# Performance work log

Hardware: AMD Instinct MI355X
Metric: run time of the kernel (lower is better)

The kernel has to match this reference:

```python
import jax, jax.numpy as jnp
import numpy as np

TAU = 1.0
EPS = 1e-5


def _gcn_sparse(x, src, dst, ew, W, b, n):
    # PyG GCNConv: add self-loops (weight 1), sym-normalize, aggregate src->dst
    deg = jax.ops.segment_sum(ew, dst, num_segments=n) + 1.0
    dinv = jnp.where(deg > 0, jax.lax.rsqrt(deg), 0.0)
    h = x @ W
    coef = dinv[src] * ew * dinv[dst]              # [E]
    out = jax.ops.segment_sum(h[src] * coef[:, None], dst, num_segments=n)
    out = out + h * (dinv * dinv)[:, None]         # self-loop term
    return out + b


def _gcn_dense(x, A, W, b):
    # x: [B,N,d], A: [B,N,N] with A[b,i,j] = weight of edge j->i
    n = A.shape[-1]
    Ah = A + jnp.eye(n, dtype=A.dtype)
    deg = Ah.sum(-1)
    dinv = jnp.where(deg > 0, jax.lax.rsqrt(deg), 0.0)
    An = dinv[:, :, None] * Ah * dinv[:, None, :]
    return jnp.einsum('bij,bjd->bid', An, x @ W) + b


def _bn_silu(x, g, be, axes):
    # BatchNorm over node axis (training-mode batch stats, biased var) + SiLU
    m = x.mean(axes, keepdims=True)
    v = x.var(axes, keepdims=True)
    return jax.nn.silu(g * (x - m) * jax.lax.rsqrt(v + EPS) + be)


def setup_inputs() -> dict:
    key = jax.random.key(0)
    ks = jax.random.split(key, 12)
    B, NPG, EPER = 32, 1024, 16384
    CIN, C, K1, K2, OUT = 64, 128, 128, 32, 10
    N, E = B * NPG, B * EPER
    ei = jax.random.randint(ks[0], (2, E), 0, NPG, dtype=jnp.int32)
    off = jnp.repeat(jnp.arange(B, dtype=jnp.int32) * NPG, EPER)
    edge_index = ei + off[None, :]
    x = jax.random.normal(ks[1], (N, CIN), jnp.float32)
    batch = jnp.repeat(jnp.arange(B, dtype=jnp.int32), NPG)
    batch_ptr = jnp.arange(B + 1, dtype=jnp.int32) * NPG
    p = lambda k, s: jax.random.normal(k, s, jnp.float32) * 0.05
    return dict(
        x=x, edge_index=edge_index, batch=batch, batch_ptr=batch_ptr,
        w1a=p(ks[2], (CIN, C)), b1a=jnp.zeros((C,)), g1a=jnp.ones((C,)), be1a=jnp.zeros((C,)),
        w1b=p(ks[3], (C, C)), b1b=jnp.zeros((C,)), g1b=jnp.ones((C,)), be1b=jnp.zeros((C,)),
        wp1=p(ks[4], (C, K1)), bp1=jnp.zeros((K1,)),
        w2a=p(ks[5], (C, C)), b2a=jnp.zeros((C,)), g2a=jnp.ones((C,)), be2a=jnp.zeros((C,)),
        w2b=p(ks[6], (C, C)), b2b=jnp.zeros((C,)), g2b=jnp.ones((C,)), be2b=jnp.zeros((C,)),
        wp2=p(ks[7], (C, K2)), bp2=jnp.zeros((K2,)),
        wl=p(ks[8], (C, OUT)), bl=jnp.zeros((OUT,)))


def reference(x, edge_index, batch, batch_ptr,
              w1a, b1a, g1a, be1a, w1b, b1b, g1b, be1b, wp1, bp1,
              w2a, b2a, g2a, be2a, w2b, b2b, g2b, be2b, wp2, bp2,
              wl, bl):
    n = x.shape[0]
    B = batch_ptr.shape[0] - 1
    npg = n // B                                    # uniform nodes per graph
    src, dst = edge_index[0], edge_index[1]
    ew = jnp.ones((edge_index.shape[1],), x.dtype)  # edge_weight=None -> ones

    # ---- stack 1: sparse GCN residual blocks + stochastic pool ----
    h = _bn_silu(_gcn_sparse(x, src, dst, ew, w1a, b1a, n), g1a, be1a, 0)
    h = h + _bn_silu(_gcn_sparse(h, src, dst, ew, w1b, b1b, n), g1b, be1b, 0)
    s = jax.nn.softmax(_gcn_sparse(h, src, dst, ew, wp1, bp1, n) / TAU, -1)  # [n,K1]
    s3 = s.reshape(B, npg, -1)
    x2 = jnp.einsum('bnc,bnd->bcd', s3, h.reshape(B, npg, -1))   # s^T x  [B,K1,C]
    t = jax.ops.segment_sum(s[src] * ew[:, None], dst, num_segments=n)  # A s
    A2 = jnp.einsum('bnc,bnk->bck', s3, t.reshape(B, npg, -1))   # s^T A s [B,K1,K1]

    # ---- stack 2: dense GCN on pooled graph + stochastic pool ----
    h2 = _bn_silu(_gcn_dense(x2, A2, w2a, b2a), g2a, be2a, (0, 1))
    h2 = h2 + _bn_silu(_gcn_dense(h2, A2, w2b, b2b), g2b, be2b, (0, 1))
    s2 = jax.nn.softmax(_gcn_dense(h2, A2, wp2, bp2) / TAU, -1)  # [B,K1,K2]
    x3 = jnp.einsum('bnc,bnd->bcd', s2, h2)                      # [B,K2,C]

    # global mean pool over nodes per graph, linear, log_softmax
    g = x3.mean(axis=1)
    out = jax.nn.log_softmax(g @ wl + bl, axis=1)
    # aux losses are multiplied by 0 in the original forward -> exact zero
    return (out, jnp.zeros((), x.dtype))
```

## Files before the change

kernel.cpp:

```cpp
#include <hip/hip_runtime.h>
#include <cmath>

#define KSPLIT 8
#define ELL_ST 80

typedef __attribute__((ext_vector_type(8))) short short8;
typedef __attribute__((ext_vector_type(4))) float float4v;

static __device__ __forceinline__ unsigned short f2bf(float f){
  union { float f; unsigned u; } c; c.f = f;
  unsigned r = c.u + 0x7fff + ((c.u >> 16) & 1);
  return (unsigned short)(r >> 16);
}
static __device__ __forceinline__ float u2f(unsigned u){
  union { unsigned u; float f; } c; c.u = u; return c.f;
}
static __device__ __forceinline__ float silu(float y){ return y/(1.f+__expf(-y)); }

static __device__ __forceinline__ void coef_prologue(const float* __restrict__ stats,
                                                     const float* __restrict__ gamma,
                                                     const float* __restrict__ beta,
                                                     float invM, float* lds, int tbase){
  int t = threadIdx.x - tbase;
  if(t >= 0 && t < 128){
    float s = 0.f, q = 0.f;
    #pragma unroll
    for(int k=0;k<8;k++){ s += stats[k*128+t]; q += stats[1024 + k*128+t]; }
    float m = s*invM;
    float v = q*invM - m*m;
    float sc = gamma[t]*rsqrtf(v + 1e-5f);
    lds[t] = sc;
    lds[128+t] = beta[t] - m*sc;
  }
}

__global__ void k_fill_wt(const int* __restrict__ src, const int* __restrict__ dst,
                          int* __restrict__ cursor, int* __restrict__ esrc, int E,
                          const float* __restrict__ w1a, const float* __restrict__ w1b,
                          const float* __restrict__ wp1, unsigned short* __restrict__ t1a,
                          unsigned short* __restrict__ t1b, unsigned short* __restrict__ tp1,
                          int CIN){
  int i = blockIdx.x*256 + threadIdx.x;
  if(i < E){
    int d = dst[i];
    int p = atomicAdd(&cursor[d], 1);
    if(p < ELL_ST) esrc[(size_t)d*ELL_ST + p] = src[i];
  } else {
    int j = i - E;
    int n1 = CIN*128, n2 = 128*128;
    if(j >= 0 && j < n1){
      int k = j >> 7, c = j & 127;
      t1a[(size_t)c*CIN + k] = f2bf(w1a[j]);
    } else if(j >= n1 && j < n1+n2){
      int jj = j - n1; int k = jj >> 7, c = jj & 127;
      t1b[(size_t)c*128 + k] = f2bf(w1b[jj]);
    } else if(j >= n1+n2 && j < n1+2*n2){
      int jj = j - n1 - n2; int k = jj >> 7, c = jj & 127;
      tp1[(size_t)c*128 + k] = f2bf(wp1[jj]);
    }
  }
}

__global__ void k_gemm_mfma(const float* __restrict__ A, const float* __restrict__ A2,
                            const unsigned short* __restrict__ Bt,
                            unsigned short* __restrict__ Cb,
                            unsigned short* __restrict__ Hout, int M, int K,
                            const int* __restrict__ rowdeg,
                            const float* __restrict__ stA, const float* __restrict__ gA,
                            const float* __restrict__ beA,
                            const float* __restrict__ stB, const float* __restrict__ gB,
                            const float* __restrict__ beB, float invM){
  __shared__ unsigned short Abf[64][40];
  __shared__ unsigned short Bbf[128][40];
  __shared__ float lcA[256], lcB[256];
  int tid = threadIdx.x;
  if(stA) coef_prologue(stA, gA, beA, invM, lcA, 0);
  if(stB) coef_prologue(stB, gB, beB, invM, lcB, 128);
  if(stA || stB) __syncthreads();
  int wv = tid >> 6, lane = tid & 63;
  int quad = lane >> 4, l16 = lane & 15;
  int row0 = blockIdx.x*64;
  int sr = tid >> 2, sk = (tid & 3)*8;
  int srb = tid >> 1, skb = (tid & 1)*16;
  float4v acc[8] = {};
  for(int kt=0; kt<K; kt+=32){
    const float* ap = &A[(size_t)(row0+sr)*K + kt + sk];
    float va[8];
    *(float4*)&va[0] = *(const float4*)ap;
    *(float4*)&va[4] = *(const float4*)(ap+4);
    if(stB){
      const float* bp = &A2[(size_t)(row0+sr)*K + kt + sk];
      float vb[8];
      *(float4*)&vb[0] = *(const float4*)bp;
      *(float4*)&vb[4] = *(const float4*)(bp+4);
      #pragma unroll
      for(int i=0;i<8;i++){
        int c = kt+sk+i;
        va[i] = silu(lcA[c]*va[i] + lcA[128+c]) + silu(lcB[c]*vb[i] + lcB[128+c]);
      }
    } else if(stA){
      #pragma unroll
      for(int i=0;i<8;i++){
        int c = kt+sk+i;
        va[i] = silu(lcA[c]*va[i] + lcA[128+c]);
      }
    }
    uint4 pk;
    pk.x = (unsigned)f2bf(va[0]) | ((unsigned)f2bf(va[1])<<16);
    pk.y = (unsigned)f2bf(va[2]) | ((unsigned)f2bf(va[3])<<16);
    pk.z = (unsigned)f2bf(va[4]) | ((unsigned)f2bf(va[5])<<16);
    pk.w = (unsigned)f2bf(va[6]) | ((unsigned)f2bf(va[7])<<16);
    *(uint4*)&Abf[sr][sk] = pk;
    if(Hout)
      *(uint4*)&Hout[(size_t)(row0+sr)*128 + kt + sk] = pk;
    *(uint4*)&Bbf[srb][skb]   = *(const uint4*)&Bt[(size_t)srb*K + kt + skb];
    *(uint4*)&Bbf[srb][skb+8] = *(const uint4*)&Bt[(size_t)srb*K + kt + skb + 8];
    __syncthreads();
    short8 af = *(const short8*)&Abf[wv*16 + l16][quad*8];
    #pragma unroll
    for(int t=0;t<8;t++){
      short8 bf = *(const short8*)&Bbf[t*16 + l16][quad*8];
      acc[t] = __builtin_amdgcn_mfma_f32_16x16x32_bf16(af, bf, acc[t], 0, 0, 0);
    }
    __syncthreads();
  }
  float scr[4];
  #pragma unroll
  for(int r=0;r<4;r++){
    int grow = row0 + wv*16 + quad*4 + r;
    scr[r] = rowdeg ? rsqrtf((float)rowdeg[grow] + 1.0f) : 1.f;
  }
  #pragma unroll
  for(int t=0;t<8;t++){
    #pragma unroll
    for(int r=0;r<4;r++){
      int grow = row0 + wv*16 + quad*4 + r;
      Cb[(size_t)grow*128 + t*16 + l16] = f2bf(acc[t][r]*scr[r]);
    }
  }
}

__global__ void k_gemm64(const float* __restrict__ A, const float* __restrict__ B,
                         float* __restrict__ C, int M, int K, int Nc,
                         const float* __restrict__ rowscale,
                         const float* __restrict__ stA, const float* __restrict__ gA,
                         const float* __restrict__ beA, float invM){
  __shared__ float As[16][68];
  __shared__ float Bs[16][68];
  __shared__ float lc[256];
  int tid = threadIdx.x;
  if(stA){ coef_prologue(stA, gA, beA, invM, lc, 0); __syncthreads(); }
  int tx = tid & 15, ty = tid >> 4;
  int row0 = blockIdx.y*64, col0 = blockIdx.x*64;
  float acc[4][4] = {};
  for(int kt=0; kt<K; kt+=16){
    int ra = tid >> 2, ka = (tid & 3)*4;
    float4 va = *(const float4*)&A[(size_t)(row0+ra)*K + kt + ka];
    if(stA){
      float vv[4] = {va.x, va.y, va.z, va.w};
      #pragma unroll
      for(int i=0;i<4;i++){
        int c = kt+ka+i;
        vv[i] = silu(lc[c]*vv[i] + lc[128+c]);
      }
      va.x=vv[0]; va.y=vv[1]; va.z=vv[2]; va.w=vv[3];
    }
    As[ka+0][ra]=va.x; As[ka+1][ra]=va.y; As[ka+2][ra]=va.z; As[ka+3][ra]=va.w;
    int rb = tid >> 4, cb = (tid & 15)*4;
    *(float4*)&Bs[rb][cb] = *(const float4*)&B[(size_t)(kt+rb)*Nc + col0 + cb];
    __syncthreads();
    #pragma unroll
    for(int k=0;k<16;k++){
      float4 a = *(const float4*)&As[k][ty*4];
      float4 b = *(const float4*)&Bs[k][tx*4];
      float av[4]={a.x,a.y,a.z,a.w}, bv[4]={b.x,b.y,b.z,b.w};
      #pragma unroll
      for(int i=0;i<4;i++)
        #pragma unroll
        for(int j=0;j<4;j++) acc[i][j] += av[i]*bv[j];
    }
    __syncthreads();
  }
  #pragma unroll
  for(int i=0;i<4;i++){
    int r = row0 + ty*4 + i;
    float sc = rowscale ? rowscale[r] : 1.0f;
    float4 v; v.x=acc[i][0]*sc; v.y=acc[i][1]*sc; v.z=acc[i][2]*sc; v.w=acc[i][3]*sc;
    *(float4*)&C[(size_t)r*Nc + col0 + tx*4] = v;
  }
}

template<bool DO_SOFTMAX, bool GCN, bool STATS, bool BF16IN, bool BF16OUT>
__global__ void k_gather(const int* __restrict__ degc, const int* __restrict__ esrc,
                         const void* __restrict__ hWs,
                         const float* __restrict__ bias, float* __restrict__ out,
                         float* __restrict__ stats){
  __shared__ float lsum[4][128];
  __shared__ float lsq[4][128];
  const unsigned short* h16 = (const unsigned short*)hWs;
  const float* h32 = (const float*)hWs;
  int wave = threadIdx.x >> 6;
  int lane = threadIdx.x & 63;
  int bid = blockIdx.x;
  int d = ((bid & 7) << 12) | ((bid >> 3) << 2) | wave;
  int grp = lane >> 5;
  int c4 = (lane & 31)*4;
  int dgr = degc[d];
  int cnt = dgr > ELL_ST ? ELL_ST : dgr;
  cnt = __builtin_amdgcn_readfirstlane(cnt);
  const int* row = esrc + (size_t)d*ELL_ST;

  auto loadrow = [&](int s)->float4{
    if(BF16IN){
      uint2 u = *(const uint2*)&h16[(size_t)s*128 + c4];
      float4 v;
      v.x = u2f(u.x << 16); v.y = u2f(u.x & 0xffff0000u);
      v.z = u2f(u.y << 16); v.w = u2f(u.y & 0xffff0000u);
      return v;
    } else {
      return *(const float4*)&h32[(size_t)s*128 + c4];
    }
  };

  float4 a0 = {0.f,0.f,0.f,0.f}, a1 = {0.f,0.f,0.f,0.f};
  float4 a2 = {0.f,0.f,0.f,0.f}, a3 = {0.f,0.f,0.f,0.f};
  if(GCN && grp == 0)
    a0 = loadrow(d);
  for(int base=0; base<cnt; base+=32){
    int m = cnt - base; if(m > 32) m = 32;
    int idx = (lane < m) ? row[base + lane] : 0;
    int full = m & ~7;
    int j0 = 0;
    for(; j0 < full; j0 += 8){
      int s0 = __shfl(idx, j0+grp);
      int s1 = __shfl(idx, j0+grp+2);
      int s2 = __shfl(idx, j0+grp+4);
      int s3 = __shfl(idx, j0+grp+6);
      float4 v0 = loadrow(s0);
      float4 v1 = loadrow(s1);
      float4 v2 = loadrow(s2);
      float4 v3 = loadrow(s3);
      a0.x+=v0.x; a0.y+=v0.y; a0.z+=v0.z; a0.w+=v0.w;
      a1.x+=v1.x; a1.y+=v1.y; a1.z+=v1.z; a1.w+=v1.w;
      a2.x+=v2.x; a2.y+=v2.y; a2.z+=v2.z; a2.w+=v2.w;
      a3.x+=v3.x; a3.y+=v3.y; a3.z+=v3.z; a3.w+=v3.w;
    }
    if(j0 < m){
      int jj0 = j0+grp, jj1 = j0+grp+2, jj2 = j0+grp+4, jj3 = j0+grp+6;
      int s0 = __shfl(idx, jj0 < m ? jj0 : 0);
      int s1 = __shfl(idx, jj1 < m ? jj1 : 0);
      int s2 = __shfl(idx, jj2 < m ? jj2 : 0);
      int s3 = __shfl(idx, jj3 < m ? jj3 : 0);
      if(jj0 < m){ float4 v = loadrow(s0);
        a0.x+=v.x; a0.y+=v.y; a0.z+=v.z; a0.w+=v.w; }
      if(jj1 < m){ float4 v = loadrow(s1);
        a1.x+=v.x; a1.y+=v.y; a1.z+=v.z; a1.w+=v.w; }
      if(jj2 < m){ float4 v = loadrow(s2);
        a2.x+=v.x; a2.y+=v.y; a2.z+=v.z; a2.w+=v.w; }
      if(jj3 < m){ float4 v = loadrow(s3);
        a3.x+=v.x; a3.y+=v.y; a3.z+=v.z; a3.w+=v.w; }
    }
  }
  float4 acc;
  acc.x = (a0.x+a1.x)+(a2.x+a3.x);
  acc.y = (a0.y+a1.y)+(a2.y+a3.y);
  acc.z = (a0.z+a1.z)+(a2.z+a3.z);
  acc.w = (a0.w+a1.w)+(a2.w+a3.w);
  acc.x += __shfl_xor(acc.x, 32);
  acc.y += __shfl_xor(acc.y, 32);
  acc.z += __shfl_xor(acc.z, 32);
  acc.w += __shfl_xor(acc.w, 32);
  float4 val = acc;
  if(GCN){
    float dv = rsqrtf((float)dgr + 1.0f);
    float4 bi = *(const float4*)&bias[c4];
    val.x = dv*acc.x + bi.x; val.y = dv*acc.y + bi.y;
    val.z = dv*acc.z + bi.z; val.w = dv*acc.w + bi.w;
  }
  if(DO_SOFTMAX){
    float mx = fmaxf(fmaxf(val.x,val.y), fmaxf(val.z,val.w));
    #pragma unroll
    for(int o=1;o<32;o<<=1) mx = fmaxf(mx, __shfl_xor(mx,o));
    float4 e; e.x=__expf(val.x-mx); e.y=__expf(val.y-mx);
    e.z=__expf(val.z-mx); e.w=__expf(val.w-mx);
    float s = e.x+e.y+e.z+e.w;
    #pragma unroll
    for(int o=1;o<32;o<<=1) s += __shfl_xor(s,o);
    float inv = 1.f/s;
    val.x=e.x*inv; val.y=e.y*inv; val.z=e.z*inv; val.w=e.w*inv;
  }
  if(grp == 0){
    if(BF16OUT){
      unsigned short* o16 = (unsigned short*)out;
      uint2 w;
      w.x = (unsigned)f2bf(val.x) | ((unsigned)f2bf(val.y)<<16);
      w.y = (unsigned)f2bf(val.z) | ((unsigned)f2bf(val.w)<<16);
      *(uint2*)&o16[(size_t)d*128 + c4] = w;
    } else {
      *(float4*)&out[(size_t)d*128 + c4] = val;
    }
  }
  if(STATS){
    if(grp == 0){
      *(float4*)&lsum[wave][c4] = val;
      float4 q; q.x=val.x*val.x; q.y=val.y*val.y; q.z=val.z*val.z; q.w=val.w*val.w;
      *(float4*)&lsq[wave][c4] = q;
    }
    __syncthreads();
    int t = threadIdx.x;
    if(t < 128){
      float s = (lsum[0][t]+lsum[1][t]) + (lsum[2][t]+lsum[3][t]);
      atomicAdd(&stats[(bid & 7)*128 + t], s);
    } else {
      int c = t - 128;
      float q = (lsq[0][c]+lsq[1][c]) + (lsq[2][c]+lsq[3][c]);
      atomicAdd(&stats[1024 + (bid & 7)*128 + c], q);
    }
  }
}

__global__ __launch_bounds__(256, 2)
void k_pool2(const unsigned short* __restrict__ P, const unsigned short* __restrict__ QH,
             const unsigned short* __restrict__ QT,
             float* __restrict__ part1, float* __restrict__ part2, int npg, int nb){
  __shared__ unsigned short sT[128][40];
  __shared__ unsigned short qT[128][40];
  int tid = threadIdx.x;
  bool zq = (blockIdx.z == 0);
  const unsigned short* Q = zq ? QH : QT;
  int ks = blockIdx.x, b = blockIdx.y;
  int klen = npg / KSPLIT;
  size_t base = ((size_t)b*npg + (size_t)ks*klen)*128;
  int wv = tid >> 6, lane = tid & 63;
  int quad = lane >> 4, l16 = lane & 15;
  int wr = (wv >> 1)*64, wc = (wv & 1)*64;
  int arr = tid >> 7;
  int t7 = tid & 127;
  int sg = (t7 >> 4)*16;
  int sr2 = (t7 & 15)*2;
  float4v acc[4][4] = {};

  for(int c0 = 0; c0 < klen; c0 += 32){
    size_t i0 = base + (size_t)(c0+sr2)*128 + sg;
    const unsigned short* Sp = arr ? Q : P;
    unsigned short (*dstT)[40] = arr ? qT : sT;
    uint4 ua = *(const uint4*)&Sp[i0];
    uint4 ub = *(const uint4*)&Sp[i0+8];
    uint4 uc = *(const uint4*)&Sp[i0+128];
    uint4 ud = *(const uint4*)&Sp[i0+136];
    unsigned short lo[16], hi[16];
    *(uint4*)&lo[0]=ua; *(uint4*)&lo[8]=ub;
    *(uint4*)&hi[0]=uc; *(uint4*)&hi[8]=ud;
    #pragma unroll
    for(int j=0;j<16;j++)
      *(unsigned*)&dstT[sg+j][sr2] = (unsigned)lo[j] | ((unsigned)hi[j]<<16);
    __syncthreads();
    #pragma unroll
    for(int i=0;i<4;i++){
      short8 af = *(const short8*)&sT[wr + i*16 + l16][quad*8];
      #pragma unroll
      for(int j=0;j<4;j++){
        short8 bf = *(const short8*)&qT[wc + j*16 + l16][quad*8];
        acc[i][j] = __builtin_amdgcn_mfma_f32_16x16x32_bf16(af, bf, acc[i][j], 0, 0, 0);
      }
    }
    __syncthreads();
  }

  float* outp = (zq ? part1 : part2) + ((size_t)(ks*nb + b)*128)*128;
  #pragma unroll
  for(int i=0;i<4;i++)
    #pragma unroll
    for(int r=0;r<4;r++){
      int m = wr + i*16 + quad*4 + r;
      #pragma unroll
      for(int j=0;j<4;j++)
        outp[(size_t)m*128 + wc + j*16 + l16] = acc[i][j][r];
    }
}

__global__ void k_pool_reduce2(const float* __restrict__ p1, const float* __restrict__ p2,
                               float* __restrict__ x2, float* __restrict__ A2,
                               float* __restrict__ dinv2, int total){
  int i = blockIdx.x*256 + threadIdx.x;
  int half = total >> 2;
  if(i < half){
    float4 s = *(const float4*)&p1[(size_t)i*4];
    #pragma unroll
    for(int ks=1; ks<KSPLIT; ks++){
      float4 v = *(const float4*)&p1[(size_t)ks*total + (size_t)i*4];
      s.x+=v.x; s.y+=v.y; s.z+=v.z; s.w+=v.w;
    }
    *(float4*)&x2[(size_t)i*4] = s;
  } else {
    int ia = i - half;
    float4 s = *(const float4*)&p2[(size_t)ia*4];
    #pragma unroll
    for(int ks=1; ks<KSPLIT; ks++){
      float4 v = *(const float4*)&p2[(size_t)ks*total + (size_t)ia*4];
      s.x+=v.x; s.y+=v.y; s.z+=v.z; s.w+=v.w;
    }
    *(float4*)&A2[(size_t)ia*4] = s;
    float rs = s.x+s.y+s.z+s.w;
    #pragma unroll
    for(int o=16;o>0;o>>=1) rs += __shfl_xor(rs, o);
    if((threadIdx.x & 31) == 0) dinv2[ia>>5] = rsqrtf(rs + 1.0f);
  }
}

__global__ void k_bgemm_post_stats(const float* __restrict__ A, const float* __restrict__ X,
                                   const float* __restrict__ dinv2, const float* __restrict__ bias,
                                   float* __restrict__ outp, float* __restrict__ stats){
  __shared__ float As[16][17], Xs[16][17];
  __shared__ float rs[16][17], rq[16][17];
  int b = blockIdx.z;
  int i0 = blockIdx.y*16, j0 = blockIdx.x*16;
  int tx = threadIdx.x, ty = threadIdx.y;
  const float* Ab = A + (size_t)b*16384;
  const float* Xb = X + (size_t)b*16384;
  float acc = 0.f;
  for(int k0=0;k0<128;k0+=16){
    As[ty][tx] = Ab[(i0+ty)*128 + k0+tx];
    Xs[ty][tx] = Xb[(k0+ty)*128 + j0+tx];
    __syncthreads();
    #pragma unroll
    for(int k=0;k<16;k++) acc += As[ty][k]*Xs[k][tx];
    __syncthreads();
  }
  int gr = b*128 + i0 + ty;
  float v = dinv2[gr]*(acc + Xb[(i0+ty)*128 + j0+tx]) + bias[j0+tx];
  outp[(size_t)gr*128 + j0+tx] = v;
  rs[ty][tx] = v; rq[ty][tx] = v*v;
  __syncthreads();
  if(ty == 0){
    float s = 0.f, q = 0.f;
    #pragma unroll
    for(int k=0;k<16;k++){ s += rs[k][tx]; q += rq[k][tx]; }
    int slot = b & 7;
    atomicAdd(&stats[slot*128 + j0+tx], s);
    atomicAdd(&stats[1024 + slot*128 + j0+tx], q);
  }
}

__global__ void k_final(const float* __restrict__ dTa, const float* __restrict__ dTb,
                        const float* __restrict__ stA, const float* __restrict__ gA,
                        const float* __restrict__ beA,
                        const float* __restrict__ stB, const float* __restrict__ gB,
                        const float* __restrict__ beB, float invMc,
                        const float* __restrict__ wl, const float* __restrict__ bl,
                        float* __restrict__ out, int K1n, int Cc, float inv_k2,
                        int OUTc, int zero_idx){
  __shared__ float lcA[256], lcB[256];
  __shared__ float red[256];
  __shared__ float gsh[128];
  __shared__ float logits[32];
  __shared__ float mred, lred;
  coef_prologue(stA, gA, beA, invMc, lcA, 0);
  coef_prologue(stB, gB, beB, invMc, lcB, 128);
  __syncthreads();
  int b = blockIdx.x;
  int tid = threadIdx.x;
  int c = tid & 127, rh = tid >> 7;
  const float* pa = dTa + (size_t)b*K1n*Cc;
  const float* pb = dTb + (size_t)b*K1n*Cc;
  float sa = lcA[c], ha = lcA[128+c], sb = lcB[c], hb = lcB[128+c];
  float acc = 0.f;
  for(int r = rh; r < K1n; r += 2){
    float ya = sa*pa[(size_t)r*Cc + c] + ha;
    float yb = sb*pb[(size_t)r*Cc + c] + hb;
    acc += silu(ya) + silu(yb);
  }
  red[tid] = acc;
  __syncthreads();
  if(tid < 128) gsh[tid] = (red[tid] + red[tid+128]) * inv_k2;
  __syncthreads();
  if(tid < OUTc){
    float l = bl[tid];
    for(int d=0; d<Cc; d++) l += gsh[d]*wl[d*OUTc + tid];
    logits[tid] = l;
  }
  __syncthreads();
  if(tid==0){
    float m = -1e30f;
    for(int o=0;o<OUTc;o++) m = fmaxf(m, logits[o]);
    float s = 0.f;
    for(int o=0;o<OUTc;o++) s += __expf(logits[o]-m);
    mred = m; lred = logf(s);
  }
  __syncthreads();
  if(tid < OUTc) out[b*OUTc + tid] = logits[tid] - mred - lred;
  if(b==0 && tid==0 && zero_idx >= 0) out[zero_idx] = 0.f;
}

extern "C" void kernel_launch(void* const* d_in, const int* in_sizes, int n_in,
                              void* d_out, int out_size, void* d_ws, size_t ws_size,
                              hipStream_t stream){
  const float* x    = (const float*)d_in[0];
  const int*   ei   = (const int*)d_in[1];
  const float* w1a  = (const float*)d_in[4];
  const float* b1a  = (const float*)d_in[5];
  const float* g1a  = (const float*)d_in[6];
  const float* be1a = (const float*)d_in[7];
  const float* w1b  = (const float*)d_in[8];
  const float* b1b  = (const float*)d_in[9];
  const float* g1b  = (const float*)d_in[10];
  const float* be1b = (const float*)d_in[11];
  const float* wp1  = (const float*)d_in[12];
  const float* bp1  = (const float*)d_in[13];
  const float* w2a  = (const float*)d_in[14];
  const float* b2a  = (const float*)d_in[15];
  const float* g2a  = (const float*)d_in[16];
  const float* be2a = (const float*)d_in[17];
  const float* w2b  = (const float*)d_in[18];
  const float* b2b  = (const float*)d_in[19];
  const float* g2b  = (const float*)d_in[20];
  const float* be2b = (const float*)d_in[21];
  const float* wl   = (const float*)d_in[24];
  const float* bl   = (const float*)d_in[25];
  float* out = (float*)d_out;

  const int C_   = in_sizes[5];
  const int CIN_ = in_sizes[4]/C_;
  const int N    = in_sizes[0]/CIN_;
  const int E    = in_sizes[1]/2;
  const int B_   = in_sizes[3]-1;
  const int NPG_ = N/B_;
  const int K1_  = in_sizes[13];
  const int K2_  = in_sizes[23];
  const int OUTc = in_sizes[25];
  const int M2   = B_*K1_;
  const int total = M2*C_;

  const int* srcI = ei;
  const int* dstI = ei + E;

  float* ws = (float*)d_ws;
  size_t o = 0;
  unsigned short* bufW = (unsigned short*)(ws + o); o += (size_t)N*C_/2;
  float* bufA  = ws + o; o += (size_t)N*C_;
  float* bufB  = ws + o; o += (size_t)N*C_;
  unsigned short* bufS = (unsigned short*)(ws + o); o += (size_t)N*C_/2;
  unsigned short* bufT = (unsigned short*)(ws + o); o += (size_t)N*C_/2;
  unsigned short* bufH = (unsigned short*)(ws + o); o += (size_t)N*C_/2;
  float* x2    = ws + o; o += (size_t)total;
  float* A2    = ws + o; o += (size_t)total;
  float* dinv2 = ws + o; o += (size_t)M2;
  float* st1a  = ws + o; o += 2048;
  float* st1b  = ws + o; o += 2048;
  float* stDa  = ws + o; o += 2048;
  float* stDb  = ws + o; o += 2048;
  int* cursor  = (int*)(ws + o); o += (size_t)N;
  float* part  = ws + o; o += (size_t)KSPLIT*total;
  float* part2 = ws + o; o += (size_t)KSPLIT*total;
  float* dW  = part;
  float* dTa = part + (size_t)total;
  float* dTb = part + 2*(size_t)total;
  unsigned short* wt1a = (unsigned short*)(ws + o); o += (size_t)CIN_*C_/2 + 64;
  unsigned short* wt1b = (unsigned short*)(ws + o); o += (size_t)C_*C_/2 + 64;
  unsigned short* wtp1 = (unsigned short*)(ws + o); o += (size_t)C_*C_/2 + 64;
  int* esrc    = (int*)(ws + o); o += (size_t)N*ELL_ST;
  (void)ws_size; (void)n_in;

  dim3 blk256(256);
  dim3 gblk(16,16);
  auto g1 = [](int n){ return dim3((unsigned)((n+255)/256)); };
  const float invN = 1.0f/N, invM2 = 1.0f/M2;

  hipMemsetAsync(st1a, 0, (size_t)4*2048*sizeof(float) + (size_t)N*sizeof(int), stream);
  k_fill_wt<<<g1(E + CIN_*C_ + 2*C_*C_), blk256, 0, stream>>>(srcI, dstI, cursor, esrc, E,
      w1a, w1b, wp1, wt1a, wt1b, wtp1, CIN_);

  dim3 gath((unsigned)(N/4));
  dim3 gmm((unsigned)(N/64));

  k_gemm_mfma<<<gmm, blk256, 0, stream>>>(x, nullptr, wt1a, bufW, nullptr, N, CIN_, cursor,
      nullptr, nullptr, nullptr, nullptr, nullptr, nullptr, 0.f);
  k_gather<false,true,true,true,false><<<gath, blk256, 0, stream>>>(cursor, esrc, bufW, b1a, bufA, st1a);

  k_gemm_mfma<<<gmm, blk256, 0, stream>>>(bufA, nullptr, wt1b, bufW, nullptr, N, C_, cursor,
      st1a, g1a, be1a, nullptr, nullptr, nullptr, invN);
  k_gather<false,true,true,true,false><<<gath, blk256, 0, stream>>>(cursor, esrc, bufW, b1b, bufB, st1b);

  k_gemm_mfma<<<gmm, blk256, 0, stream>>>(bufA, bufB, wtp1, bufW, bufH, N, C_, cursor,
      st1a, g1a, be1a, st1b, g1b, be1b, invN);
  k_gather<true,true,false,true,true><<<gath, blk256, 0, stream>>>(cursor, esrc, bufW, bp1, (float*)bufS, nullptr);
  k_gather<false,false,false,true,true><<<gath, blk256, 0, stream>>>(cursor, esrc, bufS, nullptr, (float*)bufT, nullptr);

  k_pool2<<<dim3(KSPLIT, B_, 2), blk256, 0, stream>>>(bufS, bufH, bufT,
      part, part2, NPG_, B_);
  k_pool_reduce2<<<g1(total/2), blk256, 0, stream>>>(part, part2, x2, A2, dinv2, total);

  k_gemm64<<<dim3(C_/64, M2/64), blk256, 0, stream>>>(x2, w2a, dW, M2, C_, C_, dinv2,
      nullptr, nullptr, nullptr, 0.f);
  k_bgemm_post_stats<<<dim3(C_/16, K1_/16, B_), gblk, 0, stream>>>(A2, dW, dinv2, b2a, dTa, stDa);

  k_gemm64<<<dim3(C_/64, M2/64), blk256, 0, stream>>>(dTa, w2b, dW, M2, C_, C_, dinv2,
      stDa, g2a, be2a, invM2);
  k_bgemm_post_stats<<<dim3(C_/16, K1_/16, B_), gblk, 0, stream>>>(A2, dW, dinv2, b2b, dTb, stDb);

  int zero_idx = (out_size > B_*OUTc) ? B_*OUTc : -1;
  k_final<<<dim3((unsigned)B_), blk256, 0, stream>>>(dTa, dTb,
      stDa, g2a, be2a, stDb, g2b, be2b, invM2, wl, bl, out, K1_, C_, 1.0f/K2_,
      OUTc, zero_idx);
}
```

Measured before the change: 357.9 us.

## Move dense pooled-graph GCN GEMMs to bf16 MFMA kernels

```diff
diff --git a/kernel.cpp b/kernel.cpp
--- a/kernel.cpp
+++ b/kernel.cpp
@@ -37,9 +37,11 @@
 __global__ void k_fill_wt(const int* __restrict__ src, const int* __restrict__ dst,
                           int* __restrict__ cursor, int* __restrict__ esrc, int E,
                           const float* __restrict__ w1a, const float* __restrict__ w1b,
-                          const float* __restrict__ wp1, unsigned short* __restrict__ t1a,
-                          unsigned short* __restrict__ t1b, unsigned short* __restrict__ tp1,
-                          int CIN){
+                          const float* __restrict__ wp1, const float* __restrict__ w2a,
+                          const float* __restrict__ w2b,
+                          unsigned short* __restrict__ t1a, unsigned short* __restrict__ t1b,
+                          unsigned short* __restrict__ tp1, unsigned short* __restrict__ t2a,
+                          unsigned short* __restrict__ t2b, int CIN){
   int i = blockIdx.x*256 + threadIdx.x;
   if(i < E){
     int d = dst[i];
@@ -57,6 +59,12 @@
     } else if(j >= n1+n2 && j < n1+2*n2){
       int jj = j - n1 - n2; int k = jj >> 7, c = jj & 127;
       tp1[(size_t)c*128 + k] = f2bf(wp1[jj]);
+    } else if(j >= n1+2*n2 && j < n1+3*n2){
+      int jj = j - n1 - 2*n2; int k = jj >> 7, c = jj & 127;
+      t2a[(size_t)c*128 + k] = f2bf(w2a[jj]);
+    } else if(j >= n1+3*n2 && j < n1+4*n2){
+      int jj = j - n1 - 3*n2; int k = jj >> 7, c = jj & 127;
+      t2b[(size_t)c*128 + k] = f2bf(w2b[jj]);
     }
   }
 }
@@ -66,6 +74,7 @@
                             unsigned short* __restrict__ Cb,
                             unsigned short* __restrict__ Hout, int M, int K,
                             const int* __restrict__ rowdeg,
+                            const float* __restrict__ rowscale,
                             const float* __restrict__ stA, const float* __restrict__ gA,
                             const float* __restrict__ beA,
                             const float* __restrict__ stB, const float* __restrict__ gB,
@@ -128,7 +137,7 @@
   #pragma unroll
   for(int r=0;r<4;r++){
     int grow = row0 + wv*16 + quad*4 + r;
-    scr[r] = rowdeg ? rsqrtf((float)rowdeg[grow] + 1.0f) : 1.f;
+    scr[r] = rowdeg ? rsqrtf((float)rowdeg[grow] + 1.0f) : (rowscale ? rowscale[grow] : 1.f);
   }
   #pragma unroll
   for(int t=0;t<8;t++){
@@ -137,56 +146,6 @@
       int grow = row0 + wv*16 + quad*4 + r;
       Cb[(size_t)grow*128 + t*16 + l16] = f2bf(acc[t][r]*scr[r]);
     }
-  }
-}
-
-__global__ void k_gemm64(const float* __restrict__ A, const float* __restrict__ B,
-                         float* __restrict__ C, int M, int K, int Nc,
-                         const float* __restrict__ rowscale,
-                         const float* __restrict__ stA, const float* __restrict__ gA,
-                         const float* __restrict__ beA, float invM){
-  __shared__ float As[16][68];
-  __shared__ float Bs[16][68];
-  __shared__ float lc[256];
-  int tid = threadIdx.x;
-  if(stA){ coef_prologue(stA, gA, beA, invM, lc, 0); __syncthreads(); }
-  int tx = tid & 15, ty = tid >> 4;
-  int row0 = blockIdx.y*64, col0 = blockIdx.x*64;
-  float acc[4][4] = {};
-  for(int kt=0; kt<K; kt+=16){
-    int ra = tid >> 2, ka = (tid & 3)*4;
-    float4 va = *(const float4*)&A[(size_t)(row0+ra)*K + kt + ka];
-    if(stA){
-      float vv[4] = {va.x, va.y, va.z, va.w};
-      #pragma unroll
-      for(int i=0;i<4;i++){
-        int c = kt+ka+i;
-        vv[i] = silu(lc[c]*vv[i] + lc[128+c]);
-      }
-      va.x=vv[0]; va.y=vv[1]; va.z=vv[2]; va.w=vv[3];
-    }
-    As[ka+0][ra]=va.x; As[ka+1][ra]=va.y; As[ka+2][ra]=va.z; As[ka+3][ra]=va.w;
-    int rb = tid >> 4, cb = (tid & 15)*4;
-    *(float4*)&Bs[rb][cb] = *(const float4*)&B[(size_t)(kt+rb)*Nc + col0 + cb];
-    __syncthreads();
-    #pragma unroll
-    for(int k=0;k<16;k++){
-      float4 a = *(const float4*)&As[k][ty*4];
-      float4 b = *(const float4*)&Bs[k][tx*4];
-      float av[4]={a.x,a.y,a.z,a.w}, bv[4]={b.x,b.y,b.z,b.w};
-      #pragma unroll
-      for(int i=0;i<4;i++)
-        #pragma unroll
-        for(int j=0;j<4;j++) acc[i][j] += av[i]*bv[j];
-    }
-    __syncthreads();
-  }
-  #pragma unroll
-  for(int i=0;i<4;i++){
-    int r = row0 + ty*4 + i;
-    float sc = rowscale ? rowscale[r] : 1.0f;
-    float4 v; v.x=acc[i][0]*sc; v.y=acc[i][1]*sc; v.z=acc[i][2]*sc; v.w=acc[i][3]*sc;
-    *(float4*)&C[(size_t)r*Nc + col0 + tx*4] = v;
   }
 }
 
@@ -380,7 +339,7 @@
 }
 
 __global__ void k_pool_reduce2(const float* __restrict__ p1, const float* __restrict__ p2,
-                               float* __restrict__ x2, float* __restrict__ A2,
+                               float* __restrict__ x2, unsigned short* __restrict__ A2b,
                                float* __restrict__ dinv2, int total){
   int i = blockIdx.x*256 + threadIdx.x;
   int half = total >> 2;
@@ -400,7 +359,10 @@
       float4 v = *(const float4*)&p2[(size_t)ks*total + (size_t)ia*4];
       s.x+=v.x; s.y+=v.y; s.z+=v.z; s.w+=v.w;
     }
-    *(float4*)&A2[(size_t)ia*4] = s;
+    uint2 w;
+    w.x = (unsigned)f2bf(s.x) | ((unsigned)f2bf(s.y)<<16);
+    w.y = (unsigned)f2bf(s.z) | ((unsigned)f2bf(s.w)<<16);
+    *(uint2*)&A2b[(size_t)ia*4] = w;
     float rs = s.x+s.y+s.z+s.w;
     #pragma unroll
     for(int o=16;o>0;o>>=1) rs += __shfl_xor(rs, o);
@@ -408,37 +370,85 @@
   }
 }
 
-__global__ void k_bgemm_post_stats(const float* __restrict__ A, const float* __restrict__ X,
-                                   const float* __restrict__ dinv2, const float* __restrict__ bias,
-                                   float* __restrict__ outp, float* __restrict__ stats){
-  __shared__ float As[16][17], Xs[16][17];
-  __shared__ float rs[16][17], rq[16][17];
-  int b = blockIdx.z;
-  int i0 = blockIdx.y*16, j0 = blockIdx.x*16;
-  int tx = threadIdx.x, ty = threadIdx.y;
-  const float* Ab = A + (size_t)b*16384;
-  const float* Xb = X + (size_t)b*16384;
-  float acc = 0.f;
-  for(int k0=0;k0<128;k0+=16){
-    As[ty][tx] = Ab[(i0+ty)*128 + k0+tx];
-    Xs[ty][tx] = Xb[(k0+ty)*128 + j0+tx];
+__global__ void k_bgemm_mfma(const unsigned short* __restrict__ A2b,
+                             const unsigned short* __restrict__ Xb,
+                             const float* __restrict__ dinv2, const float* __restrict__ bias,
+                             float* __restrict__ outp, float* __restrict__ stats){
+  __shared__ unsigned short Al[128][40];
+  __shared__ unsigned short Xt[128][40];
+  __shared__ float ssum[128], ssq[128];
+  int tid = threadIdx.x;
+  int b = blockIdx.x;
+  if(tid < 128){ ssum[tid] = 0.f; ssq[tid] = 0.f; }
+  int wv = tid >> 6, lane = tid & 63;
+  int quad = lane >> 4, l16 = lane & 15;
+  int wr = (wv >> 1)*64, wc = (wv & 1)*64;
+  int arr = tid >> 7;
+  int t7 = tid & 127;
+  int sg = (t7 >> 4)*16, sr2 = (t7 & 15)*2;
+  float4v acc[4][4] = {};
+
+  for(int n0 = 0; n0 < 128; n0 += 32){
+    if(arr == 0){
+      const unsigned short* ap = &A2b[((size_t)b*128 + t7)*128 + n0];
+      *(uint4*)&Al[t7][0]  = *(const uint4*)&ap[0];
+      *(uint4*)&Al[t7][8]  = *(const uint4*)&ap[8];
+      *(uint4*)&Al[t7][16] = *(const uint4*)&ap[16];
+      *(uint4*)&Al[t7][24] = *(const uint4*)&ap[24];
+    } else {
+      size_t i0 = ((size_t)(b*128 + n0 + sr2))*128 + sg;
+      uint4 ua = *(const uint4*)&Xb[i0];
+      uint4 ub = *(const uint4*)&Xb[i0+8];
+      uint4 uc = *(const uint4*)&Xb[i0+128];
+      uint4 ud = *(const uint4*)&Xb[i0+136];
+      unsigned short lo[16], hi[16];
+      *(uint4*)&lo[0]=ua; *(uint4*)&lo[8]=ub;
+      *(uint4*)&hi[0]=uc; *(uint4*)&hi[8]=ud;
+      #pragma unroll
+      for(int j=0;j<16;j++)
+        *(unsigned*)&Xt[sg+j][sr2] = (unsigned)lo[j] | ((unsigned)hi[j]<<16);
+    }
     __syncthreads();
     #pragma unroll
-    for(int k=0;k<16;k++) acc += As[ty][k]*Xs[k][tx];
+    for(int i=0;i<4;i++){
+      short8 af = *(const short8*)&Al[wr + i*16 + l16][quad*8];
+      #pragma unroll
+      for(int j=0;j<4;j++){
+        short8 bf = *(const short8*)&Xt[wc + j*16 + l16][quad*8];
+        acc[i][j] = __builtin_amdgcn_mfma_f32_16x16x32_bf16(af, bf, acc[i][j], 0, 0, 0);
+      }
+    }
     __syncthreads();
   }
-  int gr = b*128 + i0 + ty;
-  float v = dinv2[gr]*(acc + Xb[(i0+ty)*128 + j0+tx]) + bias[j0+tx];
-  outp[(size_t)gr*128 + j0+tx] = v;
-  rs[ty][tx] = v; rq[ty][tx] = v*v;
+
+  float sv[4] = {}, sq[4] = {};
+  #pragma unroll
+  for(int i=0;i<4;i++){
+    #pragma unroll
+    for(int r=0;r<4;r++){
+      int m = wr + i*16 + quad*4 + r;
+      float dv = dinv2[b*128 + m];
+      #pragma unroll
+      for(int j=0;j<4;j++){
+        int c = wc + j*16 + l16;
+        float xr = u2f((unsigned)Xb[((size_t)(b*128 + m))*128 + c] << 16);
+        float v = dv*(acc[i][j][r] + xr) + bias[c];
+        outp[((size_t)(b*128 + m))*128 + c] = v;
+        sv[j] += v; sq[j] += v*v;
+      }
+    }
+  }
+  #pragma unroll
+  for(int j=0;j<4;j++){
+    int c = wc + j*16 + l16;
+    atomicAdd(&ssum[c], sv[j]);
+    atomicAdd(&ssq[c], sq[j]);
+  }
   __syncthreads();
-  if(ty == 0){
-    float s = 0.f, q = 0.f;
-    #pragma unroll
-    for(int k=0;k<16;k++){ s += rs[k][tx]; q += rq[k][tx]; }
+  if(tid < 128){
     int slot = b & 7;
-    atomicAdd(&stats[slot*128 + j0+tx], s);
-    atomicAdd(&stats[1024 + slot*128 + j0+tx], q);
+    atomicAdd(&stats[slot*128 + tid], ssum[tid]);
+    atomicAdd(&stats[1024 + slot*128 + tid], ssq[tid]);
   }
 }
 
@@ -543,7 +553,7 @@
   unsigned short* bufT = (unsigned short*)(ws + o); o += (size_t)N*C_/2;
   unsigned short* bufH = (unsigned short*)(ws + o); o += (size_t)N*C_/2;
   float* x2    = ws + o; o += (size_t)total;
-  float* A2    = ws + o; o += (size_t)total;
+  unsigned short* A2b = (unsigned short*)(ws + o); o += (size_t)total/2;
   float* dinv2 = ws + o; o += (size_t)M2;
   float* st1a  = ws + o; o += 2048;
   float* st1b  = ws + o; o += 2048;
@@ -552,51 +562,52 @@
   int* cursor  = (int*)(ws + o); o += (size_t)N;
   float* part  = ws + o; o += (size_t)KSPLIT*total;
   float* part2 = ws + o; o += (size_t)KSPLIT*total;
-  float* dW  = part;
+  unsigned short* Xb = (unsigned short*)part;
   float* dTa = part + (size_t)total;
   float* dTb = part + 2*(size_t)total;
   unsigned short* wt1a = (unsigned short*)(ws + o); o += (size_t)CIN_*C_/2 + 64;
   unsigned short* wt1b = (unsigned short*)(ws + o); o += (size_t)C_*C_/2 + 64;
   unsigned short* wtp1 = (unsigned short*)(ws + o); o += (size_t)C_*C_/2 + 64;
+  unsigned short* wt2a = (unsigned short*)(ws + o); o += (size_t)C_*C_/2 + 64;
+  unsigned short* wt2b = (unsigned short*)(ws + o); o += (size_t)C_*C_/2 + 64;
   int* esrc    = (int*)(ws + o); o += (size_t)N*ELL_ST;
   (void)ws_size; (void)n_in;
 
   dim3 blk256(256);
-  dim3 gblk(16,16);
   auto g1 = [](int n){ return dim3((unsigned)((n+255)/256)); };
   const float invN = 1.0f/N, invM2 = 1.0f/M2;
 
   hipMemsetAsync(st1a, 0, (size_t)4*2048*sizeof(float) + (size_t)N*sizeof(int), stream);
-  k_fill_wt<<<g1(E + CIN_*C_ + 2*C_*C_), blk256, 0, stream>>>(srcI, dstI, cursor, esrc, E,
-      w1a, w1b, wp1, wt1a, wt1b, wtp1, CIN_);
+  k_fill_wt<<<g1(E + CIN_*C_ + 4*C_*C_), blk256, 0, stream>>>(srcI, dstI, cursor, esrc, E,
+      w1a, w1b, wp1, w2a, w2b, wt1a, wt1b, wtp1, wt2a, wt2b, CIN_);
 
   dim3 gath((unsigned)(N/4));
   dim3 gmm((unsigned)(N/64));
 
-  k_gemm_mfma<<<gmm, blk256, 0, stream>>>(x, nullptr, wt1a, bufW, nullptr, N, CIN_, cursor,
+  k_gemm_mfma<<<gmm, blk256, 0, stream>>>(x, nullptr, wt1a, bufW, nullptr, N, CIN_, cursor, nullptr,
       nullptr, nullptr, nullptr, nullptr, nullptr, nullptr, 0.f);
   k_gather<false,true,true,true,false><<<gath, blk256, 0, stream>>>(cursor, esrc, bufW, b1a, bufA, st1a);
 
-  k_gemm_mfma<<<gmm, blk256, 0, stream>>>(bufA, nullptr, wt1b, bufW, nullptr, N, C_, cursor,
+  k_gemm_mfma<<<gmm, blk256, 0, stream>>>(bufA, nullptr, wt1b, bufW, nullptr, N, C_, cursor, nullptr,
       st1a, g1a, be1a, nullptr, nullptr, nullptr, invN);
   k_gather<false,true,true,true,false><<<gath, blk256, 0, stream>>>(cursor, esrc, bufW, b1b, bufB, st1b);
 
-  k_gemm_mfma<<<gmm, blk256, 0, stream>>>(bufA, bufB, wtp1, bufW, bufH, N, C_, cursor,
+  k_gemm_mfma<<<gmm, blk256, 0, stream>>>(bufA, bufB, wtp1, bufW, bufH, N, C_, cursor, nullptr,
       st1a, g1a, be1a, st1b, g1b, be1b, invN);
   k_gather<true,true,false,true,true><<<gath, blk256, 0, stream>>>(cursor, esrc, bufW, bp1, (float*)bufS, nullptr);
   k_gather<false,false,false,true,true><<<gath, blk256, 0, stream>>>(cursor, esrc, bufS, nullptr, (float*)bufT, nullptr);
 
   k_pool2<<<dim3(KSPLIT, B_, 2), blk256, 0, stream>>>(bufS, bufH, bufT,
       part, part2, NPG_, B_);
-  k_pool_reduce2<<<g1(total/2), blk256, 0, stream>>>(part, part2, x2, A2, dinv2, total);
-
-  k_gemm64<<<dim3(C_/64, M2/64), blk256, 0, stream>>>(x2, w2a, dW, M2, C_, C_, dinv2,
-      nullptr, nullptr, nullptr, 0.f);
-  k_bgemm_post_stats<<<dim3(C_/16, K1_/16, B_), gblk, 0, stream>>>(A2, dW, dinv2, b2a, dTa, stDa);
-
-  k_gemm64<<<dim3(C_/64, M2/64), blk256, 0, stream>>>(dTa, w2b, dW, M2, C_, C_, dinv2,
-      stDa, g2a, be2a, invM2);
-  k_bgemm_post_stats<<<dim3(C_/16, K1_/16, B_), gblk, 0, stream>>>(A2, dW, dinv2, b2b, dTb, stDb);
+  k_pool_reduce2<<<g1(total/2), blk256, 0, stream>>>(part, part2, x2, A2b, dinv2, total);
+
+  k_gemm_mfma<<<dim3((unsigned)(M2/64)), blk256, 0, stream>>>(x2, nullptr, wt2a, Xb, nullptr,
+      M2, C_, nullptr, dinv2, nullptr, nullptr, nullptr, nullptr, nullptr, nullptr, 0.f);
+  k_bgemm_mfma<<<dim3((unsigned)B_), blk256, 0, stream>>>(A2b, Xb, dinv2, b2a, dTa, stDa);
+
+  k_gemm_mfma<<<dim3((unsigned)(M2/64)), blk256, 0, stream>>>(dTa, nullptr, wt2b, Xb, nullptr,
+      M2, C_, nullptr, dinv2, stDa, g2a, be2a, nullptr, nullptr, nullptr, invM2);
+  k_bgemm_mfma<<<dim3((unsigned)B_), blk256, 0, stream>>>(A2b, Xb, dinv2, b2b, dTb, stDb);
 
   int zero_idx = (out_size > B_*OUTc) ? B_*OUTc : -1;
   k_final<<<dim3((unsigned)B_), blk256, 0, stream>>>(dTa, dTb,
```

New measurement: 355.0 us. No clear change (-0.8%).
